# Kernel optimization log

Hardware: AMD Instinct MI355X
Metric: run time of the kernel (lower is better)

Reference implementation:

```python
import jax, jax.numpy as jnp
import numpy as np

D_MODEL = 1024
N_HEADS = 16
D_KEY = D_MODEL // N_HEADS


def setup_inputs() -> dict:
    key = jax.random.key(0)
    ks = jax.random.split(key, 11)
    s = 1.0 / np.sqrt(D_MODEL)
    inp = {
        'query': jax.random.normal(ks[0], (2, 2048, D_MODEL), dtype=jnp.float32),
        'key': jax.random.normal(ks[1], (2, 2048, D_MODEL), dtype=jnp.float32),
        'value': jax.random.normal(ks[2], (2, 2048, D_MODEL), dtype=jnp.float32),
        'Wq': jax.random.uniform(ks[3], (D_MODEL, D_MODEL), jnp.float32, -s, s),
        'bq': jax.random.uniform(ks[4], (D_MODEL,), jnp.float32, -s, s),
        'Wk': jax.random.uniform(ks[5], (D_MODEL, D_MODEL), jnp.float32, -s, s),
        'bk': jax.random.uniform(ks[6], (D_MODEL,), jnp.float32, -s, s),
        'Wv': jax.random.uniform(ks[7], (D_MODEL, D_MODEL), jnp.float32, -s, s),
        'bv': jax.random.uniform(ks[8], (D_MODEL,), jnp.float32, -s, s),
        'Wo': jax.random.uniform(ks[9], (D_MODEL, D_MODEL), jnp.float32, -s, s),
        'bo': jax.random.uniform(ks[10], (D_MODEL,), jnp.float32, -s, s),
    }
    return inp


def _split_heads(x):
    b, s, _ = x.shape
    return x.reshape(b, s, N_HEADS, D_KEY).transpose(0, 2, 1, 3)  # [b,h,s,dk]


def reference(query, key, value, Wq, bq, Wk, bk, Wv, bv, Wo, bo):
    q = _split_heads(query @ Wq.T + bq)
    k = _split_heads(key @ Wk.T + bk)
    v = _split_heads(value @ Wv.T + bv)
    scale = 1.0 / jnp.sqrt(jnp.float32(D_KEY))
    scores = jnp.einsum('bhqd,bhkd->bhqk', q, k) * scale  # [b,h,s,s]
    probs = jax.nn.softmax(scores, axis=-1)
    attn = jnp.einsum('bhqk,bhkd->bhqd', probs, v)
    b, h, s, dk = attn.shape
    combined = attn.transpose(0, 2, 1, 3).reshape(b, s, D_MODEL)
    return combined @ Wo.T + bo
```

## Files before the change

kernel.cpp:

```cpp
#include <hip/hip_runtime.h>
#include <hip/hip_bf16.h>

#define DEVI __device__ __forceinline__

typedef short bf16x8 __attribute__((ext_vector_type(8)));
typedef float f32x4  __attribute__((ext_vector_type(4)));

#define WS_XQ   0u
#define WS_XK   4194304u
#define WS_XV   8388608u
#define WS_WQ   12582912u
#define WS_WK   13631488u
#define WS_WV   14680064u
#define WS_WO   15728640u
#define WS_QB   16777216u
#define WS_KB   20971520u
#define WS_VT   25165824u
#define WS_CB   29360128u

#define QSCALE 0.18033688011112042f

DEVI short f2bf(float f) {
  union { float f; unsigned u; } c; c.f = f;
  return (short)((c.u + 0x8000u) >> 16);
}

DEVI void async16(const short* g, const short* l) {
  __builtin_amdgcn_global_load_lds(
      (const __attribute__((address_space(1))) void*)g,
      (__attribute__((address_space(3))) void*)l, 16, 0, 0);
}

__global__ __launch_bounds__(256) void conv_kernel(
    const float* __restrict__ q, const float* __restrict__ k, const float* __restrict__ v,
    const float* __restrict__ Wq, const float* __restrict__ Wk,
    const float* __restrict__ Wv, const float* __restrict__ Wo,
    short* __restrict__ ws)
{
  size_t e = ((size_t)blockIdx.x * 256 + threadIdx.x) * 4;
  const float* src; short* dst; float sc = 1.0f;
  if (e < 12582912u) {
    size_t which = e >> 22;
    size_t off   = e & 4194303u;
    src = (which == 0 ? q : which == 1 ? k : v) + off;
    dst = ws + which * 4194304u + off;
  } else {
    size_t j = e - 12582912u;
    size_t which = j >> 20;
    size_t off   = j & 1048575u;
    src = (which == 0 ? Wq : which == 1 ? Wk : which == 2 ? Wv : Wo) + off;
    dst = ws + 12582912u + which * 1048576u + off;
    if (which == 0) sc = QSCALE;
  }
  float4 f = *(const float4*)src;
  short4 o = make_short4(f2bf(f.x * sc), f2bf(f.y * sc), f2bf(f.z * sc), f2bf(f.w * sc));
  *(short4*)dst = o;
}

template <int BN>
DEVI void gemm_body(const short* __restrict__ A, const short* __restrict__ Bt,
                    const float* __restrict__ bias, void* __restrict__ C,
                    int outmode, float bscale)
{
  constexpr int Kd = 1024, Nd = 1024;
  constexpr int NT = BN / 32;
  constexpr int BI = BN / 32;
  __shared__ __attribute__((aligned(16))) short smem[8192 + BN * 64];
  short* As = smem;
  short* Bs = smem + 8192;

  const int tid  = threadIdx.x;
  const int lane = tid & 63;
  const int w    = tid >> 6;
  const int quad = lane >> 4, cl = lane & 15;
  const int m0 = blockIdx.y * 128, n0 = blockIdx.x * BN;
  const int wm = (w >> 1) * 64, wn = (w & 1) * (BN / 2);

  f32x4 acc[4][NT];
#pragma unroll
  for (int i = 0; i < 4; ++i)
#pragma unroll
    for (int j = 0; j < NT; ++j)
#pragma unroll
      for (int r = 0; r < 4; ++r) acc[i][j][r] = 0.0f;

  for (int k0 = 0; k0 < Kd; k0 += 64) {
    __syncthreads();
#pragma unroll
    for (int i = 0; i < 4; ++i) {
      int ubase = (w * 4 + i) * 64;
      int f = ubase + lane;
      int r = f >> 3;
      int kb = (f & 7) ^ (r & 7);
      async16(A + (size_t)(m0 + r) * Kd + k0 + kb * 8, As + ubase * 8);
    }
#pragma unroll
    for (int i = 0; i < BI; ++i) {
      int ubase = (w * BI + i) * 64;
      int f = ubase + lane;
      int r = f >> 3;
      int kb = (f & 7) ^ (r & 7);
      async16(Bt + (size_t)(n0 + r) * Kd + k0 + kb * 8, Bs + ubase * 8);
    }
    __builtin_amdgcn_s_waitcnt(0);
    __syncthreads();

#pragma unroll
    for (int ks = 0; ks < 2; ++ks) {
      bf16x8 af[4], bfr[NT];
#pragma unroll
      for (int mt = 0; mt < 4; ++mt) {
        int r = wm + mt * 16 + cl;
        int u = (r << 3) | (((ks << 2) | quad) ^ (r & 7));
        af[mt] = *(const bf16x8*)&As[u * 8];
      }
#pragma unroll
      for (int nt = 0; nt < NT; ++nt) {
        int r = wn + nt * 16 + cl;
        int u = (r << 3) | (((ks << 2) | quad) ^ (r & 7));
        bfr[nt] = *(const bf16x8*)&Bs[u * 8];
      }
#pragma unroll
      for (int mt = 0; mt < 4; ++mt)
#pragma unroll
        for (int nt = 0; nt < NT; ++nt)
          acc[mt][nt] = __builtin_amdgcn_mfma_f32_16x16x32_bf16(af[mt], bfr[nt], acc[mt][nt], 0, 0, 0);
    }
  }

  if (BN == 128 && outmode == 1) {
    __syncthreads();
#pragma unroll
    for (int mt = 0; mt < 4; ++mt)
#pragma unroll
      for (int nt = 0; nt < NT; ++nt) {
        int n_l = wn + nt * 16 + cl;
        float bv = bias[n0 + n_l] * bscale;
        int m_base = wm + mt * 16 + quad * 4;
        short4 pk;
        pk.x = f2bf(acc[mt][nt][0] + bv);
        pk.y = f2bf(acc[mt][nt][1] + bv);
        pk.z = f2bf(acc[mt][nt][2] + bv);
        pk.w = f2bf(acc[mt][nt][3] + bv);
        int u = m_base >> 2;
        int addr = n_l * 128 + ((u ^ (n_l & 31)) << 2);
        *(short4*)&smem[addr] = pk;
      }
    __syncthreads();
    short* Cs = (short*)C;
    int bb = m0 >> 11;
    int s0 = m0 & 2047;
#pragma unroll
    for (int p = 0; p < 4; ++p) {
      int n_l = w * 32 + p * 8 + (lane >> 3);
      int mb = (lane & 7) * 16;
      short4 t0, t1, t2, t3;
      {
        int u = (mb >> 2) + 0; t0 = *(short4*)&smem[n_l * 128 + ((u ^ (n_l & 31)) << 2)];
        u = (mb >> 2) + 1;     t1 = *(short4*)&smem[n_l * 128 + ((u ^ (n_l & 31)) << 2)];
        u = (mb >> 2) + 2;     t2 = *(short4*)&smem[n_l * 128 + ((u ^ (n_l & 31)) << 2)];
        u = (mb >> 2) + 3;     t3 = *(short4*)&smem[n_l * 128 + ((u ^ (n_l & 31)) << 2)];
      }
      size_t g = ((size_t)(bb * 1024 + n0 + n_l)) * 2048 + s0 + mb;
      *(short4*)&Cs[g]      = t0;
      *(short4*)&Cs[g + 4]  = t1;
      *(short4*)&Cs[g + 8]  = t2;
      *(short4*)&Cs[g + 12] = t3;
    }
    return;
  }

#pragma unroll
  for (int mt = 0; mt < 4; ++mt)
#pragma unroll
    for (int nt = 0; nt < NT; ++nt) {
      int n = n0 + wn + nt * 16 + cl;
      float bv = bias[n] * bscale;
#pragma unroll
      for (int r = 0; r < 4; ++r) {
        int m = m0 + wm + mt * 16 + quad * 4 + r;
        float val = acc[mt][nt][r] + bv;
        if (outmode == 2) ((float*)C)[(size_t)m * Nd + n] = val;
        else              ((short*)C)[(size_t)m * Nd + n] = f2bf(val);
      }
    }
}

__global__ __launch_bounds__(256) void proj_gemm(
    short* ws, const float* __restrict__ bq, const float* __restrict__ bk,
    const float* __restrict__ bv)
{
  int z = blockIdx.z;
  const short* A; const short* W; const float* bias; void* C;
  int mode; float bscale = 1.0f;
  if (z == 0)      { A = ws + WS_XQ; W = ws + WS_WQ; bias = bq; C = ws + WS_QB; mode = 0; bscale = QSCALE; }
  else if (z == 1) { A = ws + WS_XK; W = ws + WS_WK; bias = bk; C = ws + WS_KB; mode = 0; }
  else             { A = ws + WS_XV; W = ws + WS_WV; bias = bv; C = ws + WS_VT; mode = 1; }
  gemm_body<128>(A, W, bias, C, mode, bscale);
}

__global__ __launch_bounds__(256) void out_gemm(
    const short* __restrict__ ws, const float* __restrict__ bo, float* __restrict__ out)
{
  gemm_body<64>(ws + WS_CB, ws + WS_WO, bo, out, 2, 1.0f);
}

__global__ __launch_bounds__(256, 2) void flash_kernel(
    const short* __restrict__ Qb, const short* __restrict__ Kb,
    const short* __restrict__ Vt, short* __restrict__ comb)
{
  __shared__ __attribute__((aligned(16))) short QsPs[128 * 64];
  __shared__ __attribute__((aligned(16))) short Ks[2][64 * 64];
  __shared__ __attribute__((aligned(16))) short Vts[2][64 * 64];

  const int tid = threadIdx.x, lane = tid & 63, w = tid >> 6;
  const int quad = lane >> 4, cl = lane & 15;
  const int b = blockIdx.z, h = blockIdx.y, q0 = blockIdx.x * 128;

  const short* Qg = Qb + ((size_t)(b * 2048 + q0)) * 1024 + h * 64;
  const short* Kg = Kb + ((size_t)(b * 2048)) * 1024 + h * 64;
  const short* Vg = Vt + ((size_t)(b * 1024 + h * 64)) * 2048;

#pragma unroll
  for (int i = 0; i < 4; ++i) {
    int ubase = (w * 4 + i) * 64;
    int f = ubase + lane;
    int r = f >> 3, kb = (f & 7) ^ (r & 7);
    async16(Qg + (size_t)r * 1024 + kb * 8, QsPs + ubase * 8);
  }
#pragma unroll
  for (int i = 0; i < 2; ++i) {
    int ubase = (w * 2 + i) * 64;
    int f = ubase + lane;
    int r = f >> 3, kb = (f & 7) ^ (r & 7);
    async16(Kg + (size_t)r * 1024 + kb * 8, &Ks[0][ubase * 8]);
    async16(Vg + (size_t)r * 2048 + kb * 8, &Vts[0][ubase * 8]);
  }
  __builtin_amdgcn_s_waitcnt(0);
  __syncthreads();

  bf16x8 qa[2][2];
#pragma unroll
  for (int mt = 0; mt < 2; ++mt)
#pragma unroll
    for (int ks = 0; ks < 2; ++ks) {
      int r = w * 32 + mt * 16 + cl;
      int u = (r << 3) | (((ks << 2) | quad) ^ (r & 7));
      qa[mt][ks] = *(const bf16x8*)&QsPs[u * 8];
    }
  __syncthreads();

  f32x4 acc[2][5];
#pragma unroll
  for (int mt = 0; mt < 2; ++mt)
#pragma unroll
    for (int nt = 0; nt < 5; ++nt)
#pragma unroll
      for (int r = 0; r < 4; ++r) acc[mt][nt][r] = 0.0f;

  const bf16x8 ones = { 0x3F80, 0x3F80, 0x3F80, 0x3F80, 0x3F80, 0x3F80, 0x3F80, 0x3F80 };

  for (int jt = 0; jt < 32; ++jt) {
    const short* Kcur = Ks[jt & 1];
    const short* Vcur = Vts[jt & 1];
    if (jt < 31) {
      short* Knxt = Ks[(jt + 1) & 1];
      short* Vnxt = Vts[(jt + 1) & 1];
      int j0 = (jt + 1) * 64;
#pragma unroll
      for (int i = 0; i < 2; ++i) {
        int ubase = (w * 2 + i) * 64;
        int f = ubase + lane;
        int r = f >> 3, kb = (f & 7) ^ (r & 7);
        async16(Kg + (size_t)(j0 + r) * 1024 + kb * 8, Knxt + ubase * 8);
        async16(Vg + (size_t)r * 2048 + j0 + kb * 8, Vnxt + ubase * 8);
      }
    }

    f32x4 s[2][4];
#pragma unroll
    for (int mt = 0; mt < 2; ++mt)
#pragma unroll
      for (int nt = 0; nt < 4; ++nt)
#pragma unroll
        for (int r = 0; r < 4; ++r) s[mt][nt][r] = 0.0f;

#pragma unroll
    for (int ks = 0; ks < 2; ++ks) {
      bf16x8 ka[4];
#pragma unroll
      for (int nt = 0; nt < 4; ++nt) {
        int r = nt * 16 + cl;
        int u = (r << 3) | (((ks << 2) | quad) ^ (r & 7));
        ka[nt] = *(const bf16x8*)&Kcur[u * 8];
      }
#pragma unroll
      for (int mt = 0; mt < 2; ++mt)
#pragma unroll
        for (int nt = 0; nt < 4; ++nt)
          s[mt][nt] = __builtin_amdgcn_mfma_f32_16x16x32_bf16(qa[mt][ks], ka[nt], s[mt][nt], 0, 0, 0);
    }

#pragma unroll
    for (int mt = 0; mt < 2; ++mt)
#pragma unroll
      for (int nt = 0; nt < 4; ++nt)
#pragma unroll
        for (int r = 0; r < 4; ++r) {
          float p = __builtin_amdgcn_exp2f(s[mt][nt][r]);
          int qrow = w * 32 + mt * 16 + quad * 4 + r;
          int col = nt * 16 + cl;
          int u = (qrow << 3) | ((col >> 3) ^ (qrow & 7));
          QsPs[u * 8 + (col & 7)] = f2bf(p);
        }

#pragma unroll
    for (int kt = 0; kt < 2; ++kt) {
      bf16x8 pa[2];
#pragma unroll
      for (int mt = 0; mt < 2; ++mt) {
        int qrow = w * 32 + mt * 16 + cl;
        int u = (qrow << 3) | (((kt << 2) | quad) ^ (qrow & 7));
        pa[mt] = *(const bf16x8*)&QsPs[u * 8];
        acc[mt][4] = __builtin_amdgcn_mfma_f32_16x16x32_bf16(pa[mt], ones, acc[mt][4], 0, 0, 0);
      }
#pragma unroll
      for (int nt = 0; nt < 4; ++nt) {
        int d = nt * 16 + cl;
        int u = (d << 3) | (((kt << 2) | quad) ^ (d & 7));
        bf16x8 vb = *(const bf16x8*)&Vcur[u * 8];
#pragma unroll
        for (int mt = 0; mt < 2; ++mt)
          acc[mt][nt] = __builtin_amdgcn_mfma_f32_16x16x32_bf16(pa[mt], vb, acc[mt][nt], 0, 0, 0);
      }
    }

    __builtin_amdgcn_s_waitcnt(0);
    __syncthreads();
  }

#pragma unroll
  for (int mt = 0; mt < 2; ++mt) {
    float inv[4];
#pragma unroll
    for (int r = 0; r < 4; ++r) inv[r] = 1.0f / acc[mt][4][r];
#pragma unroll
    for (int nt = 0; nt < 4; ++nt)
#pragma unroll
      for (int r = 0; r < 4; ++r) {
        int q = q0 + w * 32 + mt * 16 + quad * 4 + r;
        int d = nt * 16 + cl;
        comb[((size_t)(b * 2048 + q)) * 1024 + h * 64 + d] = f2bf(acc[mt][nt][r] * inv[r]);
      }
  }
}

extern "C" void kernel_launch(void* const* d_in, const int* in_sizes, int n_in,
                              void* d_out, int out_size, void* d_ws, size_t ws_size,
                              hipStream_t stream) {
  const float* q  = (const float*)d_in[0];
  const float* k  = (const float*)d_in[1];
  const float* v  = (const float*)d_in[2];
  const float* Wq = (const float*)d_in[3];
  const float* bq = (const float*)d_in[4];
  const float* Wk = (const float*)d_in[5];
  const float* bk = (const float*)d_in[6];
  const float* Wv = (const float*)d_in[7];
  const float* bv = (const float*)d_in[8];
  const float* Wo = (const float*)d_in[9];
  const float* bo = (const float*)d_in[10];
  short* ws = (short*)d_ws;
  float* out = (float*)d_out;

  conv_kernel<<<16384, 256, 0, stream>>>(q, k, v, Wq, Wk, Wv, Wo, ws);
  proj_gemm<<<dim3(8, 32, 3), 256, 0, stream>>>(ws, bq, bk, bv);
  flash_kernel<<<dim3(16, 16, 2), 256, 0, stream>>>(ws + WS_QB, ws + WS_KB, ws + WS_VT, ws + WS_CB);
  out_gemm<<<dim3(16, 32), 256, 0, stream>>>(ws, bo, out);
}
```

Measured before the change: 236.3 us.

## Software-pipeline flash attention with triple-buffered KV and transposed score tiles

The flash kernel now triple-buffers K/V tiles, staging two tiles ahead, and computes the QK^T scores for the next tile before running softmax and PV on the current one, ping-ponging two score register sets. Scores are computed as K·Q so each lane holds contiguous key columns, which lets P be written to LDS as packed 8-byte stores instead of scalar shorts. The conversion kernel also handles 8 elements per thread with packed bf16 stores. This aims to overlap MFMA with exp/LDS work and cut LDS store count, at the cost of more registers and LDS, which may reduce occupancy.

```diff
diff --git a/kernel.cpp b/kernel.cpp
--- a/kernel.cpp
+++ b/kernel.cpp
@@ -25,6 +25,11 @@
   return (short)((c.u + 0x8000u) >> 16);
 }
 
+DEVI unsigned pk2(float a, float b) {
+  union { float f; unsigned u; } x, y; x.f = a; y.f = b;
+  return ((x.u + 0x8000u) >> 16) | ((y.u + 0x8000u) & 0xffff0000u);
+}
+
 DEVI void async16(const short* g, const short* l) {
   __builtin_amdgcn_global_load_lds(
       (const __attribute__((address_space(1))) void*)g,
@@ -37,7 +42,7 @@
     const float* __restrict__ Wv, const float* __restrict__ Wo,
     short* __restrict__ ws)
 {
-  size_t e = ((size_t)blockIdx.x * 256 + threadIdx.x) * 4;
+  size_t e = ((size_t)blockIdx.x * 256 + threadIdx.x) * 8;
   const float* src; short* dst; float sc = 1.0f;
   if (e < 12582912u) {
     size_t which = e >> 22;
@@ -52,9 +57,14 @@
     dst = ws + 12582912u + which * 1048576u + off;
     if (which == 0) sc = QSCALE;
   }
-  float4 f = *(const float4*)src;
-  short4 o = make_short4(f2bf(f.x * sc), f2bf(f.y * sc), f2bf(f.z * sc), f2bf(f.w * sc));
-  *(short4*)dst = o;
+  float4 f0 = *(const float4*)src;
+  float4 f1 = *(const float4*)(src + 4);
+  int4 o;
+  o.x = pk2(f0.x * sc, f0.y * sc);
+  o.y = pk2(f0.z * sc, f0.w * sc);
+  o.z = pk2(f1.x * sc, f1.y * sc);
+  o.w = pk2(f1.z * sc, f1.w * sc);
+  *(int4*)dst = o;
 }
 
 template <int BN>
@@ -209,17 +219,29 @@
     const short* __restrict__ Qb, const short* __restrict__ Kb,
     const short* __restrict__ Vt, short* __restrict__ comb)
 {
-  __shared__ __attribute__((aligned(16))) short QsPs[128 * 64];
-  __shared__ __attribute__((aligned(16))) short Ks[2][64 * 64];
-  __shared__ __attribute__((aligned(16))) short Vts[2][64 * 64];
+  __shared__ __attribute__((aligned(16))) short QsPs[8192];
+  __shared__ __attribute__((aligned(16))) short Ks[3][4096];
+  __shared__ __attribute__((aligned(16))) short Vts[3][4096];
 
   const int tid = threadIdx.x, lane = tid & 63, w = tid >> 6;
   const int quad = lane >> 4, cl = lane & 15;
   const int b = blockIdx.z, h = blockIdx.y, q0 = blockIdx.x * 128;
+  const int qrow_base = w * 32;
 
   const short* Qg = Qb + ((size_t)(b * 2048 + q0)) * 1024 + h * 64;
   const short* Kg = Kb + ((size_t)(b * 2048)) * 1024 + h * 64;
   const short* Vg = Vt + ((size_t)(b * 1024 + h * 64)) * 2048;
+
+  auto stageKV = [&](int j0, short* Kd, short* Vd) {
+#pragma unroll
+    for (int i = 0; i < 2; ++i) {
+      int ubase = (w * 2 + i) * 64;
+      int f = ubase + lane;
+      int r = f >> 3, kb = (f & 7) ^ (r & 7);
+      async16(Kg + (size_t)(j0 + r) * 1024 + kb * 8, Kd + ubase * 8);
+      async16(Vg + (size_t)r * 2048 + j0 + kb * 8, Vd + ubase * 8);
+    }
+  };
 
 #pragma unroll
   for (int i = 0; i < 4; ++i) {
@@ -228,129 +250,124 @@
     int r = f >> 3, kb = (f & 7) ^ (r & 7);
     async16(Qg + (size_t)r * 1024 + kb * 8, QsPs + ubase * 8);
   }
-#pragma unroll
-  for (int i = 0; i < 2; ++i) {
-    int ubase = (w * 2 + i) * 64;
-    int f = ubase + lane;
-    int r = f >> 3, kb = (f & 7) ^ (r & 7);
-    async16(Kg + (size_t)r * 1024 + kb * 8, &Ks[0][ubase * 8]);
-    async16(Vg + (size_t)r * 2048 + kb * 8, &Vts[0][ubase * 8]);
-  }
+  stageKV(0, Ks[0], Vts[0]);
+  stageKV(64, Ks[1], Vts[1]);
   __builtin_amdgcn_s_waitcnt(0);
+
+  bf16x8 qa[2][2];
+#pragma unroll
+  for (int qt = 0; qt < 2; ++qt)
+#pragma unroll
+    for (int ks = 0; ks < 2; ++ks) {
+      int r = qrow_base + qt * 16 + cl;
+      int off = r * 64 + ((((ks << 2) | quad) ^ (r & 7)) << 3);
+      qa[qt][ks] = *(const bf16x8*)&QsPs[off];
+    }
   __syncthreads();
 
-  bf16x8 qa[2][2];
-#pragma unroll
-  for (int mt = 0; mt < 2; ++mt)
-#pragma unroll
-    for (int ks = 0; ks < 2; ++ks) {
-      int r = w * 32 + mt * 16 + cl;
-      int u = (r << 3) | (((ks << 2) | quad) ^ (r & 7));
-      qa[mt][ks] = *(const bf16x8*)&QsPs[u * 8];
-    }
-  __syncthreads();
-
-  f32x4 acc[2][5];
-#pragma unroll
-  for (int mt = 0; mt < 2; ++mt)
-#pragma unroll
-    for (int nt = 0; nt < 5; ++nt)
-#pragma unroll
-      for (int r = 0; r < 4; ++r) acc[mt][nt][r] = 0.0f;
-
-  const bf16x8 ones = { 0x3F80, 0x3F80, 0x3F80, 0x3F80, 0x3F80, 0x3F80, 0x3F80, 0x3F80 };
-
-  for (int jt = 0; jt < 32; ++jt) {
-    const short* Kcur = Ks[jt & 1];
-    const short* Vcur = Vts[jt & 1];
-    if (jt < 31) {
-      short* Knxt = Ks[(jt + 1) & 1];
-      short* Vnxt = Vts[(jt + 1) & 1];
-      int j0 = (jt + 1) * 64;
-#pragma unroll
-      for (int i = 0; i < 2; ++i) {
-        int ubase = (w * 2 + i) * 64;
-        int f = ubase + lane;
-        int r = f >> 3, kb = (f & 7) ^ (r & 7);
-        async16(Kg + (size_t)(j0 + r) * 1024 + kb * 8, Knxt + ubase * 8);
-        async16(Vg + (size_t)r * 2048 + j0 + kb * 8, Vnxt + ubase * 8);
-      }
-    }
-
-    f32x4 s[2][4];
-#pragma unroll
-    for (int mt = 0; mt < 2; ++mt)
-#pragma unroll
-      for (int nt = 0; nt < 4; ++nt)
-#pragma unroll
-        for (int r = 0; r < 4; ++r) s[mt][nt][r] = 0.0f;
-
+  auto qk = [&](const short* Kc, f32x4 (&dst)[4][2]) {
+#pragma unroll
+    for (int m = 0; m < 4; ++m)
+#pragma unroll
+      for (int qt = 0; qt < 2; ++qt)
+#pragma unroll
+        for (int r = 0; r < 4; ++r) dst[m][qt][r] = 0.0f;
 #pragma unroll
     for (int ks = 0; ks < 2; ++ks) {
       bf16x8 ka[4];
 #pragma unroll
-      for (int nt = 0; nt < 4; ++nt) {
-        int r = nt * 16 + cl;
-        int u = (r << 3) | (((ks << 2) | quad) ^ (r & 7));
-        ka[nt] = *(const bf16x8*)&Kcur[u * 8];
-      }
-#pragma unroll
-      for (int mt = 0; mt < 2; ++mt)
-#pragma unroll
-        for (int nt = 0; nt < 4; ++nt)
-          s[mt][nt] = __builtin_amdgcn_mfma_f32_16x16x32_bf16(qa[mt][ks], ka[nt], s[mt][nt], 0, 0, 0);
-    }
-
-#pragma unroll
-    for (int mt = 0; mt < 2; ++mt)
-#pragma unroll
-      for (int nt = 0; nt < 4; ++nt)
-#pragma unroll
-        for (int r = 0; r < 4; ++r) {
-          float p = __builtin_amdgcn_exp2f(s[mt][nt][r]);
-          int qrow = w * 32 + mt * 16 + quad * 4 + r;
-          int col = nt * 16 + cl;
-          int u = (qrow << 3) | ((col >> 3) ^ (qrow & 7));
-          QsPs[u * 8 + (col & 7)] = f2bf(p);
-        }
-
+      for (int m = 0; m < 4; ++m) {
+        int r = m * 16 + cl;
+        int off = r * 64 + ((((ks << 2) | quad) ^ (r & 7)) << 3);
+        ka[m] = *(const bf16x8*)&Kc[off];
+      }
+#pragma unroll
+      for (int m = 0; m < 4; ++m)
+#pragma unroll
+        for (int qt = 0; qt < 2; ++qt)
+          dst[m][qt] = __builtin_amdgcn_mfma_f32_16x16x32_bf16(ka[m], qa[qt][ks], dst[m][qt], 0, 0, 0);
+    }
+  };
+
+  f32x4 sA[4][2], sB[4][2];
+  f32x4 accO[2][4];
+  f32x4 accL[2];
+#pragma unroll
+  for (int qt = 0; qt < 2; ++qt) {
+#pragma unroll
+    for (int r = 0; r < 4; ++r) accL[qt][r] = 0.0f;
+#pragma unroll
+    for (int d = 0; d < 4; ++d)
+#pragma unroll
+      for (int r = 0; r < 4; ++r) accO[qt][d][r] = 0.0f;
+  }
+
+  const bf16x8 ones = { 0x3F80, 0x3F80, 0x3F80, 0x3F80, 0x3F80, 0x3F80, 0x3F80, 0x3F80 };
+
+  qk(Ks[0], sA);
+
+  auto body = [&](int j, f32x4 (&cur)[4][2], f32x4 (&nxt)[4][2]) {
+    if (j + 2 < 32) {
+      int bi = (j + 2) % 3;
+      stageKV((j + 2) * 64, Ks[bi], Vts[bi]);
+    }
+    if (j + 1 < 32) qk(Ks[(j + 1) % 3], nxt);
+#pragma unroll
+    for (int ksub = 0; ksub < 4; ++ksub)
+#pragma unroll
+      for (int qt = 0; qt < 2; ++qt) {
+        int qrow = qrow_base + qt * 16 + cl;
+        int u = ksub * 2 + (quad >> 1);
+        int off = qrow * 64 + ((u ^ (qrow & 7)) << 3) + ((quad & 1) << 2);
+        int2 pk;
+        pk.x = pk2(__builtin_amdgcn_exp2f(cur[ksub][qt][0]),
+                   __builtin_amdgcn_exp2f(cur[ksub][qt][1]));
+        pk.y = pk2(__builtin_amdgcn_exp2f(cur[ksub][qt][2]),
+                   __builtin_amdgcn_exp2f(cur[ksub][qt][3]));
+        *(int2*)&QsPs[off] = pk;
+      }
+    const short* Vc = Vts[j % 3];
 #pragma unroll
     for (int kt = 0; kt < 2; ++kt) {
       bf16x8 pa[2];
 #pragma unroll
-      for (int mt = 0; mt < 2; ++mt) {
-        int qrow = w * 32 + mt * 16 + cl;
-        int u = (qrow << 3) | (((kt << 2) | quad) ^ (qrow & 7));
-        pa[mt] = *(const bf16x8*)&QsPs[u * 8];
-        acc[mt][4] = __builtin_amdgcn_mfma_f32_16x16x32_bf16(pa[mt], ones, acc[mt][4], 0, 0, 0);
-      }
-#pragma unroll
-      for (int nt = 0; nt < 4; ++nt) {
-        int d = nt * 16 + cl;
-        int u = (d << 3) | (((kt << 2) | quad) ^ (d & 7));
-        bf16x8 vb = *(const bf16x8*)&Vcur[u * 8];
-#pragma unroll
-        for (int mt = 0; mt < 2; ++mt)
-          acc[mt][nt] = __builtin_amdgcn_mfma_f32_16x16x32_bf16(pa[mt], vb, acc[mt][nt], 0, 0, 0);
-      }
-    }
-
+      for (int qt = 0; qt < 2; ++qt) {
+        int qrow = qrow_base + qt * 16 + cl;
+        int off = qrow * 64 + ((((kt << 2) | quad) ^ (qrow & 7)) << 3);
+        pa[qt] = *(const bf16x8*)&QsPs[off];
+        accL[qt] = __builtin_amdgcn_mfma_f32_16x16x32_bf16(pa[qt], ones, accL[qt], 0, 0, 0);
+      }
+#pragma unroll
+      for (int d = 0; d < 4; ++d) {
+        int r = d * 16 + cl;
+        int off = r * 64 + ((((kt << 2) | quad) ^ (r & 7)) << 3);
+        bf16x8 vb = *(const bf16x8*)&Vc[off];
+#pragma unroll
+        for (int qt = 0; qt < 2; ++qt)
+          accO[qt][d] = __builtin_amdgcn_mfma_f32_16x16x32_bf16(pa[qt], vb, accO[qt][d], 0, 0, 0);
+      }
+    }
     __builtin_amdgcn_s_waitcnt(0);
     __syncthreads();
-  }
-
-#pragma unroll
-  for (int mt = 0; mt < 2; ++mt) {
+  };
+
+  for (int j = 0; j < 32; j += 2) {
+    body(j, sA, sB);
+    body(j + 1, sB, sA);
+  }
+
+#pragma unroll
+  for (int qt = 0; qt < 2; ++qt) {
     float inv[4];
 #pragma unroll
-    for (int r = 0; r < 4; ++r) inv[r] = 1.0f / acc[mt][4][r];
-#pragma unroll
-    for (int nt = 0; nt < 4; ++nt)
+    for (int r = 0; r < 4; ++r) inv[r] = 1.0f / accL[qt][r];
+#pragma unroll
+    for (int d = 0; d < 4; ++d)
 #pragma unroll
       for (int r = 0; r < 4; ++r) {
-        int q = q0 + w * 32 + mt * 16 + quad * 4 + r;
-        int d = nt * 16 + cl;
-        comb[((size_t)(b * 2048 + q)) * 1024 + h * 64 + d] = f2bf(acc[mt][nt][r] * inv[r]);
+        int q = q0 + qrow_base + qt * 16 + quad * 4 + r;
+        int dc = d * 16 + cl;
+        comb[((size_t)(b * 2048 + q)) * 1024 + h * 64 + dc] = f2bf(accO[qt][d][r] * inv[r]);
       }
   }
 }
@@ -372,7 +389,7 @@
   short* ws = (short*)d_ws;
   float* out = (float*)d_out;
 
-  conv_kernel<<<16384, 256, 0, stream>>>(q, k, v, Wq, Wk, Wv, Wo, ws);
+  conv_kernel<<<8192, 256, 0, stream>>>(q, k, v, Wq, Wk, Wv, Wo, ws);
   proj_gemm<<<dim3(8, 32, 3), 256, 0, stream>>>(ws, bq, bk, bv);
   flash_kernel<<<dim3(16, 16, 2), 256, 0, stream>>>(ws + WS_QB, ws + WS_KB, ws + WS_VT, ws + WS_CB);
   out_gemm<<<dim3(16, 32), 256, 0, stream>>>(ws, bo, out);
```

Measured after the change: 227.0 us. 1.04x faster.
